# Optimization experiments

Measured on AMD Instinct MI355X. Metric: run time of the kernel, lower is better.

## Reference

```python
import jax, jax.numpy as jnp
import numpy as np

B, S, HID = 2, 4096, 2048
NH, NKV, HD = 32, 8, 64
GROUPS = NH // NKV
ROPE_THETA = 10000.0


def _rope_cos_sin(seq_len, dim, dtype):
    inv_freq = 1.0 / (ROPE_THETA ** (jnp.arange(0, dim, 2, dtype=jnp.float32) / dim))
    pos = jnp.arange(seq_len, dtype=jnp.float32)
    freqs = pos[:, None] * inv_freq[None, :]          # [S, D/2]
    emb = jnp.concatenate([freqs, freqs], axis=-1)    # [S, D]
    return jnp.cos(emb).astype(dtype), jnp.sin(emb).astype(dtype)


def _rotate_half(x):
    x1, x2 = jnp.split(x, 2, axis=-1)
    return jnp.concatenate([-x2, x1], axis=-1)


def _apply_rope(x, cos, sin):
    # x: [B, H, S, D]; cos/sin: [S, D]
    return x * cos[None, None] + _rotate_half(x) * sin[None, None]


def kappa(x):
    return jax.nn.elu(x) + 1.0


def setup_inputs() -> dict:
    key = jax.random.key(0)
    ks = jax.random.split(key, 6)
    sc = 0.02
    return {
        "hidden_states": jax.random.normal(ks[0], (B, S, HID), jnp.float32),
        "Wq": jax.random.normal(ks[1], (HID, NH * HD), jnp.float32) * sc,
        "Wk": jax.random.normal(ks[2], (HID, NKV * HD), jnp.float32) * sc,
        "Wv": jax.random.normal(ks[3], (HID, NKV * HD), jnp.float32) * sc,
        "Wphi": jax.random.normal(ks[4], (HID, HID), jnp.float32) * sc,
        "Wo": jax.random.normal(ks[5], (HID, HID), jnp.float32) * sc,
    }


def reference(hidden_states, Wq, Wk, Wv, Wphi, Wo):
    bsz, q_len, _ = hidden_states.shape

    q = (hidden_states @ Wq).reshape(bsz, q_len, NH, HD).transpose(0, 2, 1, 3)   # [B,NH,S,D]
    k = (hidden_states @ Wk).reshape(bsz, q_len, NKV, HD).transpose(0, 2, 1, 3)  # [B,NKV,S,D]
    v = (hidden_states @ Wv).reshape(bsz, q_len, NKV, HD).transpose(0, 2, 1, 3)

    cos, sin = _rope_cos_sin(q_len, HD, hidden_states.dtype)
    q = _apply_rope(q, cos, sin)
    k = _apply_rope(k, cos, sin)

    # repeat_kv for GQA: [B,NKV,S,D] -> [B,NH,S,D]
    k = jnp.repeat(k, GROUPS, axis=1)
    v = jnp.repeat(v, GROUPS, axis=1)

    Qk = kappa(q)   # [B,NH,S,D]
    Kk = kappa(k)

    Qg = Qk.mean(axis=2)                                # [B,NH,D] global query
    logits = jnp.einsum("bnd,bnsd->bns", Qg, Kk)        # [B,NH,S]
    alpha = jax.nn.softmax(logits, axis=-1) * float(q_len)

    # KV aggregation: [B,NH,D,D] state
    outer_sum = jnp.einsum("bns,bnsd,bnsf->bndf", alpha, Kk, v)
    result_attn = jnp.einsum("bnsd,bndf->bnsf", Qk, outer_sum)  # [B,NH,S,D]

    X_phi = (hidden_states @ Wphi).reshape(bsz, q_len, NH, HD).transpose(0, 2, 1, 3)
    ctx = (X_phi * result_attn).transpose(0, 2, 1, 3).reshape(bsz, q_len, HID)
    return ctx @ Wo
```

## Files before the change

### kernel.cpp

```cpp
#include <hip/hip_runtime.h>
#include <hip/hip_bf16.h>

#define B_ 2
#define S_ 4096
#define HID_ 2048
#define NH_ 32
#define NKV_ 8
#define HD_ 64
#define GROUPS_ 4
#define NCH_ 32

typedef short short8 __attribute__((ext_vector_type(8)));
typedef float floatx4 __attribute__((ext_vector_type(4)));

__device__ __forceinline__ float bf2f(unsigned short u){
  union { unsigned int i; float f; } v; v.i = ((unsigned int)u) << 16; return v.f;
}
__device__ __forceinline__ unsigned short f2bf(float f){
  union { float f; unsigned int i; } v; v.f = f;
  unsigned int i = v.i;
  unsigned int r = (i + 0x7fffu + ((i >> 16) & 1u)) >> 16;
  return (unsigned short)r;
}

__device__ __forceinline__ void async_copy16(unsigned short* lds, const unsigned short* g){
  __builtin_amdgcn_global_load_lds((const __attribute__((address_space(1))) void*)g,
                                   (__attribute__((address_space(3))) void*)lds,
                                   16, 0, 0);
}

__global__ void conv_bf16(const float* __restrict__ x, unsigned short* __restrict__ y, int n4){
  int i = blockIdx.x * 256 + threadIdx.x;
  if (i < n4){
    float4 v = ((const float4*)x)[i];
    ushort4 o;
    o.x = f2bf(v.x); o.y = f2bf(v.y); o.z = f2bf(v.z); o.w = f2bf(v.w);
    ((ushort4*)y)[i] = o;
  }
}

__global__ void transpose_to_bf16(const float* __restrict__ W, unsigned short* __restrict__ Wt,
                                  int K, int N){
  __shared__ float tile[32][33];
  int n0 = blockIdx.x * 32, k0 = blockIdx.y * 32;
  int tx = threadIdx.x, ty = threadIdx.y;
  #pragma unroll
  for (int j = 0; j < 4; j++)
    tile[ty + j*8][tx] = W[(size_t)(k0 + ty + j*8) * N + n0 + tx];
  __syncthreads();
  #pragma unroll
  for (int j = 0; j < 4; j++)
    Wt[(size_t)(n0 + ty + j*8) * K + k0 + tx] = f2bf(tile[tx][ty + j*8]);
}

#define GTILE 16384

__global__ __launch_bounds__(512, 2) void gemm256(
    const unsigned short* __restrict__ A, const unsigned short* __restrict__ Bt,
    float* __restrict__ C, int M, int N, int K)
{
  __shared__ __align__(16) unsigned short As[2 * GTILE];
  __shared__ __align__(16) unsigned short Bs[2 * GTILE];

  const int tid = threadIdx.x;
  const int w = tid >> 6, lane = tid & 63;
  const int wr = w >> 2, wc = w & 3;
  const int l15 = lane & 15, quad = lane >> 4;

  const int nbx = N >> 8;
  int flat = blockIdx.y * nbx + blockIdx.x;
  int nwg  = nbx * (M >> 8);
  int cpx  = nwg >> 3;
  int swz  = (flat & 7) * cpx + (flat >> 3);
  int bx = swz % nbx, by = swz / nbx;
  const int m0 = by << 8, n0 = bx << 8;

  const int srow = (w << 3) + (lane >> 3);
  const int scc  = (lane & 7) ^ (lane >> 3);
  const unsigned short* gA = A  + (size_t)(m0 + srow) * K + scc * 8;
  const unsigned short* gB = Bt + (size_t)(n0 + srow) * K + scc * 8;
  const size_t rs64  = (size_t)64  * K;
  const size_t rs128 = (size_t)128 * K;
  unsigned short* lA0 = As + (w << 9);
  unsigned short* lB0 = Bs + (w << 9);

#define STAGE_A(bsel, h, t) do { \
    unsigned short* _d = lA0 + (bsel) * GTILE + (h) * 8192; \
    const unsigned short* _g = gA + (size_t)(h) * rs128 + (size_t)(t) * 64; \
    async_copy16(_d, _g); \
    async_copy16(_d + 4096, _g + rs64); \
  } while (0)
#define STAGE_B(bsel, h, t) do { \
    unsigned short* _d = lB0 + (bsel) * GTILE + (h) * 8192; \
    const unsigned short* _g = gB + (size_t)(h) * rs128 + (size_t)(t) * 64; \
    async_copy16(_d, _g); \
    async_copy16(_d + 4096, _g + rs64); \
  } while (0)
#define SCHED0 __builtin_amdgcn_sched_barrier(0)

  const int ks0  = ((quad     ^ (lane & 7)) << 3);
  const int ks1  = (((4+quad) ^ (lane & 7)) << 3);
  const int arow = (wr * 128 + l15) * 64;
  const int brow = (wc * 64  + l15) * 64;

  floatx4 acc[8][4] = {};
  short8 af[8][2], bfr[4][2];

  const int nt = K >> 6;

  STAGE_A(0, 0, 0); STAGE_A(0, 1, 0); STAGE_B(0, 0, 0); STAGE_B(0, 1, 0);
  if (nt > 1){
    STAGE_A(1, 0, 1); STAGE_A(1, 1, 1); STAGE_B(1, 0, 1); STAGE_B(1, 1, 1);
    asm volatile("s_waitcnt vmcnt(8)" ::: "memory");
  } else {
    asm volatile("s_waitcnt vmcnt(0)" ::: "memory");
  }
  SCHED0;
  __builtin_amdgcn_s_barrier();
  SCHED0;

  for (int T = 0; T < nt; ++T){
    const int cb = T & 1;
    const unsigned short* Ab = As + cb * GTILE;
    const unsigned short* Bb = Bs + cb * GTILE;

    #pragma unroll
    for (int m = 0; m < 4; ++m){
      af[m][0] = *(const short8*)(Ab + arow + m * 1024 + ks0);
      af[m][1] = *(const short8*)(Ab + arow + m * 1024 + ks1);
    }
    #pragma unroll
    for (int n = 0; n < 2; ++n){
      bfr[n][0] = *(const short8*)(Bb + brow + n * 1024 + ks0);
      bfr[n][1] = *(const short8*)(Bb + brow + n * 1024 + ks1);
    }
    SCHED0; __builtin_amdgcn_s_barrier(); SCHED0;
    __builtin_amdgcn_s_setprio(1);
    #pragma unroll
    for (int m = 0; m < 4; ++m)
      #pragma unroll
      for (int n = 0; n < 2; ++n){
        acc[m][n] = __builtin_amdgcn_mfma_f32_16x16x32_bf16(af[m][0], bfr[n][0], acc[m][n], 0, 0, 0);
        acc[m][n] = __builtin_amdgcn_mfma_f32_16x16x32_bf16(af[m][1], bfr[n][1], acc[m][n], 0, 0, 0);
      }
    __builtin_amdgcn_s_setprio(0);
    SCHED0; __builtin_amdgcn_s_barrier(); SCHED0;

    #pragma unroll
    for (int m = 0; m < 4; ++m){
      af[4+m][0] = *(const short8*)(Ab + arow + (4+m) * 1024 + ks0);
      af[4+m][1] = *(const short8*)(Ab + arow + (4+m) * 1024 + ks1);
    }
    #pragma unroll
    for (int n = 0; n < 2; ++n){
      bfr[2+n][0] = *(const short8*)(Bb + brow + (2+n) * 1024 + ks0);
      bfr[2+n][1] = *(const short8*)(Bb + brow + (2+n) * 1024 + ks1);
    }
    SCHED0; __builtin_amdgcn_s_barrier(); SCHED0;
    __builtin_amdgcn_s_setprio(1);
    #pragma unroll
    for (int m = 0; m < 4; ++m)
      #pragma unroll
      for (int n = 0; n < 2; ++n){
        acc[m][2+n] = __builtin_amdgcn_mfma_f32_16x16x32_bf16(af[m][0], bfr[2+n][0], acc[m][2+n], 0, 0, 0);
        acc[m][2+n] = __builtin_amdgcn_mfma_f32_16x16x32_bf16(af[m][1], bfr[2+n][1], acc[m][2+n], 0, 0, 0);
      }
    __builtin_amdgcn_s_setprio(0);
    SCHED0; __builtin_amdgcn_s_barrier(); SCHED0;

    if (T + 2 < nt){ STAGE_A(cb, 0, T + 2); STAGE_A(cb, 1, T + 2); }
    SCHED0; __builtin_amdgcn_s_barrier(); SCHED0;
    __builtin_amdgcn_s_setprio(1);
    #pragma unroll
    for (int m = 0; m < 4; ++m)
      #pragma unroll
      for (int n = 0; n < 2; ++n){
        acc[4+m][n] = __builtin_amdgcn_mfma_f32_16x16x32_bf16(af[4+m][0], bfr[n][0], acc[4+m][n], 0, 0, 0);
        acc[4+m][n] = __builtin_amdgcn_mfma_f32_16x16x32_bf16(af[4+m][1], bfr[n][1], acc[4+m][n], 0, 0, 0);
      }
    __builtin_amdgcn_s_setprio(0);
    SCHED0; __builtin_amdgcn_s_barrier(); SCHED0;

    if (T + 2 < nt){
      STAGE_B(cb, 0, T + 2); STAGE_B(cb, 1, T + 2);
      asm volatile("s_waitcnt vmcnt(8)" ::: "memory");
    } else {
      asm volatile("s_waitcnt vmcnt(0)" ::: "memory");
    }
    SCHED0; __builtin_amdgcn_s_barrier(); SCHED0;
    __builtin_amdgcn_s_setprio(1);
    #pragma unroll
    for (int m = 0; m < 4; ++m)
      #pragma unroll
      for (int n = 0; n < 2; ++n){
        acc[4+m][2+n] = __builtin_amdgcn_mfma_f32_16x16x32_bf16(af[4+m][0], bfr[2+n][0], acc[4+m][2+n], 0, 0, 0);
        acc[4+m][2+n] = __builtin_amdgcn_mfma_f32_16x16x32_bf16(af[4+m][1], bfr[2+n][1], acc[4+m][2+n], 0, 0, 0);
      }
    __builtin_amdgcn_s_setprio(0);
    SCHED0; __builtin_amdgcn_s_barrier(); SCHED0;
  }

#undef STAGE_A
#undef STAGE_B
#undef SCHED0

  #pragma unroll
  for (int mi = 0; mi < 8; ++mi){
    const int row = m0 + wr * 128 + mi * 16 + quad * 4;
    #pragma unroll
    for (int ni = 0; ni < 4; ++ni){
      const int col = n0 + wc * 64 + ni * 16 + l15;
      #pragma unroll
      for (int r = 0; r < 4; ++r)
        C[(size_t)(row + r) * N + col] = acc[mi][ni][r];
    }
  }
}

__global__ void rope_kappa_q(const float* __restrict__ Qlin, unsigned short* __restrict__ Qk){
  int idx = blockIdx.x * 256 + threadIdx.x;
  int i = idx & 31;
  int n = (idx >> 5) & (NH_ - 1);
  int s = (idx >> 10) & (S_ - 1);
  int b = idx >> 22;
  float invf = exp2f(-(float)i * (13.287712379549449f / 32.0f));
  float ang = (float)s * invf;
  float c = cosf(ang), sn = sinf(ang);
  size_t in_o = ((size_t)(b * S_ + s) * NH_ + n) * HD_;
  float x1 = Qlin[in_o + i];
  float x2 = Qlin[in_o + i + 32];
  float r1 = x1 * c - x2 * sn;
  float r2 = x2 * c + x1 * sn;
  r1 = r1 > 0.f ? r1 + 1.f : __expf(r1);
  r2 = r2 > 0.f ? r2 + 1.f : __expf(r2);
  size_t o = ((size_t)(b * NH_ + n) * S_ + s) * HD_;
  Qk[o + i] = f2bf(r1);
  Qk[o + i + 32] = f2bf(r2);
}

__global__ void rope_kappa_k(const float* __restrict__ KVlin, unsigned short* __restrict__ Kk){
  int idx = blockIdx.x * 256 + threadIdx.x;
  int i = idx & 31;
  int kv = (idx >> 5) & (NKV_ - 1);
  int s = (idx >> 8) & (S_ - 1);
  int b = idx >> 20;
  float invf = exp2f(-(float)i * (13.287712379549449f / 32.0f));
  float ang = (float)s * invf;
  float c = cosf(ang), sn = sinf(ang);
  size_t in_o = (size_t)(b * S_ + s) * 1024 + kv * HD_;
  float x1 = KVlin[in_o + i];
  float x2 = KVlin[in_o + i + 32];
  float r1 = x1 * c - x2 * sn;
  float r2 = x2 * c + x1 * sn;
  r1 = r1 > 0.f ? r1 + 1.f : __expf(r1);
  r2 = r2 > 0.f ? r2 + 1.f : __expf(r2);
  size_t o = ((size_t)(b * NKV_ + kv) * S_ + s) * HD_;
  Kk[o + i] = f2bf(r1);
  Kk[o + i + 32] = f2bf(r2);
}

__global__ __launch_bounds__(256) void qg_mean(const unsigned short* __restrict__ Qk,
                                               float* __restrict__ Qg){
  int bn = blockIdx.x, chunk = blockIdx.y;
  int tid = threadIdx.x;
  int dgrp = tid & 7, sgrp = tid >> 3;
  const unsigned short* base = Qk + (size_t)bn * S_ * HD_
                             + (size_t)(chunk * 256 + sgrp) * HD_ + dgrp * 8;
  float acc[8] = {};
  #pragma unroll
  for (int i = 0; i < 8; i++){
    short8 v = *(const short8*)(base + (size_t)i * 32 * HD_);
    #pragma unroll
    for (int e = 0; e < 8; e++) acc[e] += bf2f((unsigned short)v[e]);
  }
  __shared__ float red[256][8];
  #pragma unroll
  for (int e = 0; e < 8; e++) red[tid][e] = acc[e];
  __syncthreads();
  if (tid < 64){
    int dg = tid >> 3, e = tid & 7;
    float s = 0.f;
    #pragma unroll
    for (int g = 0; g < 32; g++) s += red[g * 8 + dg][e];
    atomicAdd(&Qg[bn * 64 + tid], s * (1.0f / (float)S_));
  }
}

__global__ __launch_bounds__(256) void logits_kernel(const unsigned short* __restrict__ Kk,
                                                     const float* __restrict__ Qg,
                                                     float* __restrict__ logits){
  int bn = blockIdx.x, chunk = blockIdx.y;
  int b = bn / NH_, n = bn % NH_, kv = n / GROUPS_;
  int tid = threadIdx.x;
  __shared__ float qg[64];
  if (tid < 64) qg[tid] = Qg[bn * 64 + tid];
  __syncthreads();
  int s = chunk * 256 + tid;
  const unsigned short* row = Kk + ((size_t)(b * NKV_ + kv) * S_ + s) * HD_;
  float acc = 0.f;
  #pragma unroll
  for (int c = 0; c < 8; c++){
    short8 v = *(const short8*)(row + c * 8);
    #pragma unroll
    for (int e = 0; e < 8; e++) acc += qg[c * 8 + e] * bf2f((unsigned short)v[e]);
  }
  logits[(size_t)bn * S_ + s] = acc;
}

__global__ __launch_bounds__(256) void softmax_kernel(const float* __restrict__ logits,
                                                      float* __restrict__ alpha){
  int bn = blockIdx.x;
  int tid = threadIdx.x;
  float l[16];
  float mymax = -1e30f;
  #pragma unroll
  for (int j = 0; j < 16; j++){
    l[j] = logits[(size_t)bn * S_ + j * 256 + tid];
    mymax = fmaxf(mymax, l[j]);
  }
  __shared__ float red[256];
  red[tid] = mymax; __syncthreads();
  for (int st = 128; st > 0; st >>= 1){
    if (tid < st) red[tid] = fmaxf(red[tid], red[tid + st]);
    __syncthreads();
  }
  float gmax = red[0];
  __syncthreads();
  float mysum = 0.f;
  #pragma unroll
  for (int j = 0; j < 16; j++){ l[j] = __expf(l[j] - gmax); mysum += l[j]; }
  red[tid] = mysum; __syncthreads();
  for (int st = 128; st > 0; st >>= 1){
    if (tid < st) red[tid] += red[tid + st];
    __syncthreads();
  }
  float inv = (float)S_ / red[0];
  #pragma unroll
  for (int j = 0; j < 16; j++)
    alpha[(size_t)bn * S_ + j * 256 + tid] = l[j] * inv;
}

__global__ __launch_bounds__(256) void outer_sum_kernel(const unsigned short* __restrict__ Kk,
                                                        const float* __restrict__ KVlin,
                                                        const float* __restrict__ alpha,
                                                        float* __restrict__ part){
  int bkv = blockIdx.x, chunk = blockIdx.y;
  int b = bkv >> 3, kv = bkv & 7;
  int tid = threadIdx.x;
  int d = tid >> 2, fb = (tid & 3) * 16;
  __shared__ float ks[64][64];
  __shared__ float vs[64][64];
  __shared__ float as[4][64];
  float acc[4][16] = {};
  const unsigned short* kb = Kk + (size_t)(b * NKV_ + kv) * S_ * HD_;
  const int SPC = S_ / NCH_;

  for (int t = 0; t < SPC / 64; t++){
    int ss = chunk * SPC + t * 64;
    #pragma unroll
    for (int j = 0; j < 16; j++){
      int idx = j * 256 + tid;
      int si = idx >> 6, dd = idx & 63;
      ks[si][dd] = bf2f(kb[(size_t)(ss + si) * HD_ + dd]);
      vs[si][dd] = KVlin[(size_t)(b * S_ + ss + si) * 1024 + 512 + kv * HD_ + dd];
    }
    {
      int h = tid >> 6, si = tid & 63;
      as[h][si] = alpha[(size_t)(b * NH_ + kv * GROUPS_ + h) * S_ + ss + si];
    }
    __syncthreads();
    #pragma unroll 4
    for (int si = 0; si < 64; si++){
      float k = ks[si][d];
      float4 v0 = *(const float4*)&vs[si][fb];
      float4 v1 = *(const float4*)&vs[si][fb + 4];
      float4 v2 = *(const float4*)&vs[si][fb + 8];
      float4 v3 = *(const float4*)&vs[si][fb + 12];
      #pragma unroll
      for (int h = 0; h < 4; h++){
        float ak = as[h][si] * k;
        acc[h][0]  += ak * v0.x; acc[h][1]  += ak * v0.y; acc[h][2]  += ak * v0.z; acc[h][3]  += ak * v0.w;
        acc[h][4]  += ak * v1.x; acc[h][5]  += ak * v1.y; acc[h][6]  += ak * v1.z; acc[h][7]  += ak * v1.w;
        acc[h][8]  += ak * v2.x; acc[h][9]  += ak * v2.y; acc[h][10] += ak * v2.z; acc[h][11] += ak * v2.w;
        acc[h][12] += ak * v3.x; acc[h][13] += ak * v3.y; acc[h][14] += ak * v3.z; acc[h][15] += ak * v3.w;
      }
    }
    __syncthreads();
  }

  #pragma unroll
  for (int h = 0; h < 4; h++){
    float* pb = part + ((size_t)(chunk * 16 + bkv) * 4 + h) * 4096 + d * 64 + fb;
    #pragma unroll
    for (int j = 0; j < 4; j++)
      *(float4*)&pb[j * 4] = *(float4*)&acc[h][j * 4];
  }
}

__global__ __launch_bounds__(256) void osum_reduce(const float* __restrict__ part,
                                                   float* __restrict__ osum){
  int i = blockIdx.x * 256 + threadIdx.x;
  float4 s = {0.f, 0.f, 0.f, 0.f};
  #pragma unroll 8
  for (int c = 0; c < NCH_; c++){
    float4 v = ((const float4*)part)[(size_t)c * 65536 + i];
    s.x += v.x; s.y += v.y; s.z += v.z; s.w += v.w;
  }
  ((float4*)osum)[i] = s;
}

__global__ __launch_bounds__(256) void ctx_kernel(const unsigned short* __restrict__ Qk,
                                                  const float* __restrict__ osum,
                                                  const float* __restrict__ Xphi,
                                                  unsigned short* __restrict__ ctx){
  int bn = blockIdx.x, sc = blockIdx.y;
  int b = bn / NH_, n = bn % NH_;
  int tid = threadIdx.x;
  __shared__ float os[64][65];
  __shared__ float qs[64][65];
  #pragma unroll
  for (int j = 0; j < 16; j++){
    int idx = j * 256 + tid;
    int r = idx >> 6, cix = idx & 63;
    os[r][cix] = osum[(size_t)bn * 4096 + idx];
    qs[r][cix] = bf2f(Qk[((size_t)bn * S_ + sc * 64 + r) * HD_ + cix]);
  }
  __syncthreads();
  int sl = tid >> 2, fb = (tid & 3) * 16;
  float r[16] = {};
  #pragma unroll 8
  for (int d = 0; d < 64; d++){
    float q = qs[sl][d];
    #pragma unroll
    for (int j = 0; j < 16; j++) r[j] += q * os[d][fb + j];
  }
  int s = sc * 64 + sl;
  const float* xp = Xphi + ((size_t)(b * S_ + s) * NH_ + n) * HD_ + fb;
  unsigned short* cp = ctx + (size_t)(b * S_ + s) * HID_ + n * HD_ + fb;
  #pragma unroll
  for (int j = 0; j < 16; j++) cp[j] = f2bf(xp[j] * r[j]);
}

extern "C" void kernel_launch(void* const* d_in, const int* in_sizes, int n_in,
                              void* d_out, int out_size, void* d_ws, size_t ws_size,
                              hipStream_t stream) {
  const float* hs   = (const float*)d_in[0];
  const float* Wq   = (const float*)d_in[1];
  const float* Wk   = (const float*)d_in[2];
  const float* Wv   = (const float*)d_in[3];
  const float* Wphi = (const float*)d_in[4];
  const float* Wo   = (const float*)d_in[5];
  float* out = (float*)d_out;

  char* ws = (char*)d_ws;
  const size_t M = (size_t)B_ * S_;
  size_t off = 0;
  auto alloc = [&](size_t bytes){ size_t o = off; off += (bytes + 255) & ~(size_t)255; return o; };

  size_t off_hsb   = alloc(M * HID_ * 2);
  size_t off_wqt   = alloc((size_t)HID_ * HID_ * 2);
  size_t off_wkvt  = alloc((size_t)HID_ * 1024 * 2);
  size_t off_wpt   = alloc((size_t)HID_ * HID_ * 2);
  size_t off_wot   = alloc((size_t)HID_ * HID_ * 2);
  size_t off_qlin  = alloc(M * HID_ * 4);
  size_t off_kvlin = alloc(M * 1024 * 4);
  size_t off_qk    = alloc(M * HID_ * 2);
  size_t off_kk    = alloc(M * 512 * 2);
  size_t off_qg    = alloc(64 * 64 * 4);
  size_t off_alph  = alloc((size_t)B_ * NH_ * S_ * 4);
  size_t off_osum  = alloc((size_t)B_ * NH_ * 4096 * 4);
  size_t off_ctx   = off_kvlin;
  size_t off_part  = off_qlin;
  (void)ws_size;

  unsigned short* hsb  = (unsigned short*)(ws + off_hsb);
  unsigned short* wqt  = (unsigned short*)(ws + off_wqt);
  unsigned short* wkvt = (unsigned short*)(ws + off_wkvt);
  unsigned short* wpt  = (unsigned short*)(ws + off_wpt);
  unsigned short* wot  = (unsigned short*)(ws + off_wot);
  float* qlin  = (float*)(ws + off_qlin);
  float* kvlin = (float*)(ws + off_kvlin);
  unsigned short* qk = (unsigned short*)(ws + off_qk);
  unsigned short* kk = (unsigned short*)(ws + off_kk);
  float* qg   = (float*)(ws + off_qg);
  float* alph = (float*)(ws + off_alph);
  float* osum = (float*)(ws + off_osum);
  float* part = (float*)(ws + off_part);
  unsigned short* ctx = (unsigned short*)(ws + off_ctx);

  conv_bf16<<<(int)(M * HID_ / 4 / 256), 256, 0, stream>>>(hs, hsb, (int)(M * HID_ / 4));
  transpose_to_bf16<<<dim3(HID_/32, HID_/32), dim3(32,8), 0, stream>>>(Wq, wqt, HID_, HID_);
  transpose_to_bf16<<<dim3(512/32,  HID_/32), dim3(32,8), 0, stream>>>(Wk, wkvt, HID_, 512);
  transpose_to_bf16<<<dim3(512/32,  HID_/32), dim3(32,8), 0, stream>>>(Wv, wkvt + (size_t)512 * HID_, HID_, 512);
  transpose_to_bf16<<<dim3(HID_/32, HID_/32), dim3(32,8), 0, stream>>>(Wphi, wpt, HID_, HID_);
  transpose_to_bf16<<<dim3(HID_/32, HID_/32), dim3(32,8), 0, stream>>>(Wo, wot, HID_, HID_);
  gemm256<<<dim3(HID_/256, M/256), 512, 0, stream>>>(hsb, wqt, qlin, (int)M, HID_, HID_);
  gemm256<<<dim3(1024/256, M/256), 512, 0, stream>>>(hsb, wkvt, kvlin, (int)M, 1024, HID_);
  rope_kappa_q<<<(int)(M * NH_ * 32 / 256), 256, 0, stream>>>(qlin, qk);
  rope_kappa_k<<<(int)(M * NKV_ * 32 / 256), 256, 0, stream>>>(kvlin, kk);
  hipMemsetAsync(qg, 0, 64 * 64 * 4, stream);
  qg_mean<<<dim3(B_ * NH_, S_ / 256), 256, 0, stream>>>(qk, qg);
  logits_kernel<<<dim3(B_ * NH_, S_ / 256), 256, 0, stream>>>(kk, qg, alph);
  softmax_kernel<<<B_ * NH_, 256, 0, stream>>>(alph, alph);
  outer_sum_kernel<<<dim3(B_ * NKV_, NCH_), 256, 0, stream>>>(kk, kvlin, alph, part);
  osum_reduce<<<256, 256, 0, stream>>>(part, osum);
  gemm256<<<dim3(HID_/256, M/256), 512, 0, stream>>>(hsb, wpt, qlin, (int)M, HID_, HID_);
  ctx_kernel<<<dim3(B_ * NH_, S_ / 64), 256, 0, stream>>>(qk, osum, qlin, ctx);
  gemm256<<<dim3(HID_/256, M/256), 512, 0, stream>>>(ctx, wot, out, (int)M, HID_, HID_);
}
```

Baseline: 632.0 us.

## Compute ctx with bf16 MFMA using split hi/lo transposed osum

After: 567.0 us. 1.11x faster.

```diff
diff --git a/kernel.cpp b/kernel.cpp
--- a/kernel.cpp
+++ b/kernel.cpp
@@ -397,48 +397,95 @@
   }
 }
 
-__global__ __launch_bounds__(256) void osum_reduce(const float* __restrict__ part,
-                                                   float* __restrict__ osum){
-  int i = blockIdx.x * 256 + threadIdx.x;
-  float4 s = {0.f, 0.f, 0.f, 0.f};
-  #pragma unroll 8
-  for (int c = 0; c < NCH_; c++){
-    float4 v = ((const float4*)part)[(size_t)c * 65536 + i];
-    s.x += v.x; s.y += v.y; s.z += v.z; s.w += v.w;
-  }
-  ((float4*)osum)[i] = s;
-}
-
-__global__ __launch_bounds__(256) void ctx_kernel(const unsigned short* __restrict__ Qk,
-                                                  const float* __restrict__ osum,
-                                                  const float* __restrict__ Xphi,
-                                                  unsigned short* __restrict__ ctx){
-  int bn = blockIdx.x, sc = blockIdx.y;
-  int b = bn / NH_, n = bn % NH_;
+__global__ __launch_bounds__(256) void osum_reduce_t(const float* __restrict__ part,
+                                                     unsigned short* __restrict__ osumb){
+  int bn = blockIdx.x;
   int tid = threadIdx.x;
   __shared__ float os[64][65];
-  __shared__ float qs[64][65];
+  const float4* p4 = (const float4*)part;
+  #pragma unroll
+  for (int r = 0; r < 4; r++){
+    int idx4 = r * 256 + tid;
+    float4 s = {0.f, 0.f, 0.f, 0.f};
+    #pragma unroll 8
+    for (int c = 0; c < NCH_; c++){
+      float4 v = p4[(size_t)c * 65536 + bn * 1024 + idx4];
+      s.x += v.x; s.y += v.y; s.z += v.z; s.w += v.w;
+    }
+    int d = idx4 >> 4;
+    int f0 = (idx4 & 15) * 4;
+    os[d][f0] = s.x; os[d][f0+1] = s.y; os[d][f0+2] = s.z; os[d][f0+3] = s.w;
+  }
+  __syncthreads();
+  int f = tid >> 2, d0 = (tid & 3) * 16;
+  unsigned short hi[16], lo[16];
   #pragma unroll
   for (int j = 0; j < 16; j++){
-    int idx = j * 256 + tid;
-    int r = idx >> 6, cix = idx & 63;
-    os[r][cix] = osum[(size_t)bn * 4096 + idx];
-    qs[r][cix] = bf2f(Qk[((size_t)bn * S_ + sc * 64 + r) * HD_ + cix]);
-  }
-  __syncthreads();
-  int sl = tid >> 2, fb = (tid & 3) * 16;
-  float r[16] = {};
-  #pragma unroll 8
-  for (int d = 0; d < 64; d++){
-    float q = qs[sl][d];
-    #pragma unroll
-    for (int j = 0; j < 16; j++) r[j] += q * os[d][fb + j];
-  }
-  int s = sc * 64 + sl;
-  const float* xp = Xphi + ((size_t)(b * S_ + s) * NH_ + n) * HD_ + fb;
-  unsigned short* cp = ctx + (size_t)(b * S_ + s) * HID_ + n * HD_ + fb;
-  #pragma unroll
-  for (int j = 0; j < 16; j++) cp[j] = f2bf(xp[j] * r[j]);
+    float x = os[d0 + j][f];
+    unsigned short h = f2bf(x);
+    hi[j] = h;
+    lo[j] = f2bf(x - bf2f(h));
+  }
+  unsigned short* oh = osumb + ((size_t)bn * 2) * 4096 + (size_t)f * 64 + d0;
+  unsigned short* ol = oh + 4096;
+  *(short8*)(oh)     = *(const short8*)(hi);
+  *(short8*)(oh + 8) = *(const short8*)(hi + 8);
+  *(short8*)(ol)     = *(const short8*)(lo);
+  *(short8*)(ol + 8) = *(const short8*)(lo + 8);
+}
+
+__global__ __launch_bounds__(256) void ctx_mfma(const unsigned short* __restrict__ Qk,
+                                                const unsigned short* __restrict__ osumb,
+                                                const float* __restrict__ Xphi,
+                                                unsigned short* __restrict__ ctx){
+  int bn = blockIdx.x, sc = blockIdx.y;
+  int b = bn >> 5, n = bn & 31;
+  int tid = threadIdx.x;
+  int w = tid >> 6, lane = tid & 63;
+  int l15 = lane & 15, quad = lane >> 4;
+
+  const unsigned short* obase = osumb + ((size_t)bn * 2) * 4096;
+  short8 bh[4][2], bl[4][2];
+  #pragma unroll
+  for (int nf = 0; nf < 4; nf++){
+    int f = nf * 16 + l15;
+    #pragma unroll
+    for (int kh = 0; kh < 2; kh++){
+      bh[nf][kh] = *(const short8*)(obase + (size_t)f * 64 + kh * 32 + quad * 8);
+      bl[nf][kh] = *(const short8*)(obase + 4096 + (size_t)f * 64 + kh * 32 + quad * 8);
+    }
+  }
+
+  int s0 = sc * 256 + w * 64;
+  const unsigned short* qbase = Qk + ((size_t)bn * S_ + s0) * HD_;
+  floatx4 acc[4][4] = {};
+  #pragma unroll
+  for (int m = 0; m < 4; m++){
+    short8 a0 = *(const short8*)(qbase + (size_t)(m * 16 + l15) * HD_ + quad * 8);
+    short8 a1 = *(const short8*)(qbase + (size_t)(m * 16 + l15) * HD_ + 32 + quad * 8);
+    #pragma unroll
+    for (int nf = 0; nf < 4; nf++){
+      acc[m][nf] = __builtin_amdgcn_mfma_f32_16x16x32_bf16(a0, bh[nf][0], acc[m][nf], 0, 0, 0);
+      acc[m][nf] = __builtin_amdgcn_mfma_f32_16x16x32_bf16(a1, bh[nf][1], acc[m][nf], 0, 0, 0);
+      acc[m][nf] = __builtin_amdgcn_mfma_f32_16x16x32_bf16(a0, bl[nf][0], acc[m][nf], 0, 0, 0);
+      acc[m][nf] = __builtin_amdgcn_mfma_f32_16x16x32_bf16(a1, bl[nf][1], acc[m][nf], 0, 0, 0);
+    }
+  }
+
+  #pragma unroll
+  for (int m = 0; m < 4; m++){
+    #pragma unroll
+    for (int r = 0; r < 4; r++){
+      int s = s0 + m * 16 + quad * 4 + r;
+      const float* xp = Xphi + ((size_t)(b * S_ + s) * NH_ + n) * HD_;
+      unsigned short* cp = ctx + (size_t)(b * S_ + s) * HID_ + n * HD_;
+      #pragma unroll
+      for (int nf = 0; nf < 4; nf++){
+        int f = nf * 16 + l15;
+        cp[f] = f2bf(xp[f] * acc[m][nf][r]);
+      }
+    }
+  }
 }
 
 extern "C" void kernel_launch(void* const* d_in, const int* in_sizes, int n_in,
@@ -468,7 +515,7 @@
   size_t off_kk    = alloc(M * 512 * 2);
   size_t off_qg    = alloc(64 * 64 * 4);
   size_t off_alph  = alloc((size_t)B_ * NH_ * S_ * 4);
-  size_t off_osum  = alloc((size_t)B_ * NH_ * 4096 * 4);
+  size_t off_osumb = alloc((size_t)64 * 2 * 4096 * 2);
   size_t off_ctx   = off_kvlin;
   size_t off_part  = off_qlin;
   (void)ws_size;
@@ -484,7 +531,7 @@
   unsigned short* kk = (unsigned short*)(ws + off_kk);
   float* qg   = (float*)(ws + off_qg);
   float* alph = (float*)(ws + off_alph);
-  float* osum = (float*)(ws + off_osum);
+  unsigned short* osumb = (unsigned short*)(ws + off_osumb);
   float* part = (float*)(ws + off_part);
   unsigned short* ctx = (unsigned short*)(ws + off_ctx);
 
@@ -503,8 +550,8 @@
   logits_kernel<<<dim3(B_ * NH_, S_ / 256), 256, 0, stream>>>(kk, qg, alph);
   softmax_kernel<<<B_ * NH_, 256, 0, stream>>>(alph, alph);
   outer_sum_kernel<<<dim3(B_ * NKV_, NCH_), 256, 0, stream>>>(kk, kvlin, alph, part);
-  osum_reduce<<<256, 256, 0, stream>>>(part, osum);
+  osum_reduce_t<<<64, 256, 0, stream>>>(part, osumb);
   gemm256<<<dim3(HID_/256, M/256), 512, 0, stream>>>(hsb, wpt, qlin, (int)M, HID_, HID_);
-  ctx_kernel<<<dim3(B_ * NH_, S_ / 64), 256, 0, stream>>>(qk, osum, qlin, ctx);
+  ctx_mfma<<<dim3(B_ * NH_, S_ / 64 / 4), 256, 0, stream>>>(qk, osumb, qlin, ctx);
   gemm256<<<dim3(HID_/256, M/256), 512, 0, stream>>>(ctx, wot, out, (int)M, HID_, HID_);
 }
```
